# Kernel optimization log

Hardware: AMD Instinct MI355X
Metric: run time of the kernel (lower is better)

The kernel has to match this reference:

```python
import jax, jax.numpy as jnp
import numpy as np

EPS = 1e-3


def interpolate_dim(x, n_out):
    # linear interpolation along axis 1, align_corners=True (matches F.interpolate linear)
    n_in = x.shape[1]
    pos = jnp.linspace(0.0, n_in - 1.0, n_out)
    idx0 = jnp.floor(pos).astype(jnp.int32)
    idx1 = jnp.minimum(idx0 + 1, n_in - 1)
    w = (pos - idx0.astype(x.dtype))[None, :, None]
    return x[:, idx0] * (1.0 - w) + x[:, idx1] * w


def logits_to_a_coeff(a_logits, eps):
    # stability-triangle parameterization: |a1| < 2, |a1| - 1 < a2 < 1
    stab = 1.0 - eps
    a1 = 2.0 * jnp.tanh(a_logits[..., 0]) * stab
    a1_abs = jnp.abs(a1)
    a2 = 0.5 * ((2.0 - a1_abs) * jnp.tanh(a_logits[..., 1]) * stab + a1_abs)
    return jnp.stack([a1, a2], axis=-1)  # (B, T, 2)


def sample_wise_lpc(x, a_coeff):
    # time-varying all-pole: y[t] = x[t] - a1[t]*y[t-1] - a2[t]*y[t-2]
    bs = x.shape[0]
    xs = (x.T, a_coeff[..., 0].T, a_coeff[..., 1].T)  # (T, B) each

    def step(carry, inp):
        y1, y2 = carry
        xt, a1, a2 = inp
        y = xt - a1 * y1 - a2 * y2
        return (y, y1), y

    zero = jnp.zeros((bs,), x.dtype)
    _, ys = jax.lax.scan(step, (zero, zero), xs)
    return ys.T  # (B, T)


def time_varying_fir(y, b_coeff):
    # y_out[t] = b0[t]*y[t] + b1[t]*y[t-1] + b2[t]*y[t-2], zero initial conditions
    y_pad = jnp.pad(y, ((0, 0), (2, 0)))
    return (b_coeff[..., 0] * y
            + b_coeff[..., 1] * y_pad[:, 1:-1]
            + b_coeff[..., 2] * y_pad[:, :-2])


def setup_inputs() -> dict:
    key = jax.random.key(0)
    k1, k2 = jax.random.split(key)
    x = jax.random.normal(k1, (32, 262144), dtype=jnp.float32)
    coeff_logits = jax.random.normal(k2, (32, 256, 5), dtype=jnp.float32)
    return {"x": x, "coeff_logits": coeff_logits}


def reference(x, coeff_logits):
    n_samples = x.shape[1]
    # interp_coeff=False: interpolate logits to sample rate first
    logits = interpolate_dim(coeff_logits, n_samples)  # (B, n_samples, 5)
    a_coeff = logits_to_a_coeff(logits[..., :2], EPS)  # (B, n_samples, 2)
    b_coeff = logits[..., 2:]                          # (B, n_samples, 3)
    y_a = sample_wise_lpc(x, a_coeff)
    y_ab = time_varying_fir(y_a, b_coeff)
    return y_ab
```

## Files before the change

### kernel.cpp

```cpp
#include <hip/hip_runtime.h>
#include <math.h>

#define BATCH 32
#define NSAMP 262144
#define NKNOT 256
#define EPSV  0.001f
#define CH    16
#define CPB   256
#define NCROW (NSAMP / CH)
#define BPR   (NCROW / CPB)
#define NB    (BATCH * BPR)
#define TC    (NB * CPB)
#define NWAVE (CPB / 64)

__device__ __forceinline__ float fast_tanh(float x) {
    float e = __expf(2.0f * x);
    float r = __builtin_amdgcn_rcpf(e + 1.0f);
    return fmaf(-2.0f, r, 1.0f);
}

__global__ __launch_bounds__(256, 4) void k_agg(
    const float* __restrict__ x,
    const float* __restrict__ cl,
    float* __restrict__ Cb,
    float* __restrict__ G)
{
    __shared__ float wag[NWAVE][6];
    const int tid = threadIdx.x;
    const int b = blockIdx.x;
    const int lane = tid & 63, wid = tid >> 6;

    int chunk = b * CPB + tid;
    const float4* xp = (const float4*)(x + (size_t)chunk * CH);

    int r = chunk >> 14;
    int c = chunk & (NCROW - 1);
    const float scale = 255.0f / 262143.0f;
    float pos0 = (float)(c * CH) * scale;
    float fiA = floorf(pos0);
    int idxA = (int)fiA;
    float w0v = pos0 - fiA;
    const float* kb = cl + (size_t)r * NKNOT * 5;
    int i1 = min(idxA + 1, NKNOT - 1);
    int i2 = min(idxA + 2, NKNOT - 1);
    float k00 = kb[idxA*5+0], k01 = kb[i1*5+0], k02 = kb[i2*5+0];
    float k10 = kb[idxA*5+1], k11 = kb[i1*5+1], k12 = kb[i2*5+1];
    float d0A = k01-k00, d0B = k02-k01;
    float d1A = k11-k10, d1B = k12-k11;

    const float stab = 1.0f - EPSV, stab2 = 2.0f * stab;
    float p1 = 0.f, p2 = 0.f, A1 = 1.f, A2 = 0.f, B1 = 0.f, B2 = 1.f;
    #pragma unroll
    for (int v4 = 0; v4 < 4; ++v4) {
        float4 xq = xp[v4];
        #pragma unroll
        for (int q = 0; q < 4; ++q) {
            int j = v4 * 4 + q;
            float w = fmaf((float)j, scale, w0v);
            bool sel = w >= 1.0f;
            float wu = sel ? w - 1.0f : w;
            float l0 = fmaf(wu, sel ? d0B : d0A, sel ? k01 : k00);
            float l1 = fmaf(wu, sel ? d1B : d1A, sel ? k11 : k10);
            float a1 = stab2 * fast_tanh(l0);
            float a1a = fabsf(a1);
            float a2 = 0.5f * fmaf((2.0f - a1a) * stab, fast_tanh(l1), a1a);
            float p  = fmaf(-a2, p2, (&xq.x)[q]);  p = fmaf(-a1, p1, p);
            float hA = fmaf(-a1, A1, -a2 * A2);
            float hB = fmaf(-a1, B1, -a2 * B2);
            p2 = p1; p1 = p;
            A2 = A1; A1 = hA;
            B2 = B1; B1 = hB;
        }
    }
    float L00 = A1, L01 = B1, L10 = A2, L11 = B2, Lv0 = p1, Lv1 = p2;

    #pragma unroll
    for (int d = 1; d < 64; d <<= 1) {
        float o00 = __shfl_up(L00, d), o01 = __shfl_up(L01, d);
        float o10 = __shfl_up(L10, d), o11 = __shfl_up(L11, d);
        float ov0 = __shfl_up(Lv0, d), ov1 = __shfl_up(Lv1, d);
        if (lane >= d) {
            float n00 = L00 * o00 + L01 * o10;
            float n01 = L00 * o01 + L01 * o11;
            float n10 = L10 * o00 + L11 * o10;
            float n11 = L10 * o01 + L11 * o11;
            float nv0 = fmaf(L00, ov0, fmaf(L01, ov1, Lv0));
            float nv1 = fmaf(L10, ov0, fmaf(L11, ov1, Lv1));
            L00 = n00; L01 = n01; L10 = n10; L11 = n11; Lv0 = nv0; Lv1 = nv1;
        }
    }
    if (lane == 63) {
        wag[wid][0] = L00; wag[wid][1] = L01; wag[wid][2] = L10;
        wag[wid][3] = L11; wag[wid][4] = Lv0; wag[wid][5] = Lv1;
    }
    __syncthreads();

    float P00 = 1.f, P01 = 0.f, P10 = 0.f, P11 = 1.f, Pv0 = 0.f, Pv1 = 0.f;
    for (int w2 = 0; w2 < wid; ++w2) {
        float a00 = wag[w2][0], a01 = wag[w2][1], a10 = wag[w2][2];
        float a11 = wag[w2][3], av0 = wag[w2][4], av1 = wag[w2][5];
        float n00 = a00 * P00 + a01 * P10;
        float n01 = a00 * P01 + a01 * P11;
        float n10 = a10 * P00 + a11 * P10;
        float n11 = a10 * P01 + a11 * P11;
        float nv0 = fmaf(a00, Pv0, fmaf(a01, Pv1, av0));
        float nv1 = fmaf(a10, Pv0, fmaf(a11, Pv1, av1));
        P00 = n00; P01 = n01; P10 = n10; P11 = n11; Pv0 = nv0; Pv1 = nv1;
    }
    float E00 = __shfl_up(L00, 1), E01 = __shfl_up(L01, 1);
    float E10 = __shfl_up(L10, 1), E11 = __shfl_up(L11, 1);
    float Ev0 = __shfl_up(Lv0, 1), Ev1 = __shfl_up(Lv1, 1);
    if (lane == 0) { E00 = 1.f; E01 = 0.f; E10 = 0.f; E11 = 1.f; Ev0 = 0.f; Ev1 = 0.f; }
    Cb[0*TC + chunk] = E00 * P00 + E01 * P10;
    Cb[1*TC + chunk] = E00 * P01 + E01 * P11;
    Cb[2*TC + chunk] = E10 * P00 + E11 * P10;
    Cb[3*TC + chunk] = E10 * P01 + E11 * P11;
    Cb[4*TC + chunk] = fmaf(E00, Pv0, fmaf(E01, Pv1, Ev0));
    Cb[5*TC + chunk] = fmaf(E10, Pv0, fmaf(E11, Pv1, Ev1));

    if (tid == CPB - 1) {
        G[0*NB + b] = L00 * P00 + L01 * P10;
        G[1*NB + b] = L00 * P01 + L01 * P11;
        G[2*NB + b] = L10 * P00 + L11 * P10;
        G[3*NB + b] = L10 * P01 + L11 * P11;
        G[4*NB + b] = fmaf(L00, Pv0, fmaf(L01, Pv1, Lv0));
        G[5*NB + b] = fmaf(L10, Pv0, fmaf(L11, Pv1, Lv1));
    }
}

__global__ __launch_bounds__(256, 6) void k_apply(
    const float* __restrict__ x,
    const float* __restrict__ cl,
    const float* __restrict__ Cb,
    const float* __restrict__ G,
    float* __restrict__ out)
{
    __shared__ float sInit[2];
    const int tid = threadIdx.x;
    const int b = blockIdx.x;
    const int lane = tid & 63, wid = tid >> 6;

    if (wid == 0) {
        int rowFirst = b & ~(BPR - 1);
        int k = rowFirst + lane;
        float A00 = G[0*NB + k], A01 = G[1*NB + k], A10 = G[2*NB + k];
        float A11 = G[3*NB + k], Av0 = G[4*NB + k], Av1 = G[5*NB + k];
        #pragma unroll
        for (int d = 1; d < 64; d <<= 1) {
            float o00 = __shfl_up(A00, d), o01 = __shfl_up(A01, d);
            float o10 = __shfl_up(A10, d), o11 = __shfl_up(A11, d);
            float ov0 = __shfl_up(Av0, d), ov1 = __shfl_up(Av1, d);
            if (lane >= d) {
                float n00 = A00 * o00 + A01 * o10;
                float n01 = A00 * o01 + A01 * o11;
                float n10 = A10 * o00 + A11 * o10;
                float n11 = A10 * o01 + A11 * o11;
                float nv0 = fmaf(A00, ov0, fmaf(A01, ov1, Av0));
                float nv1 = fmaf(A10, ov0, fmaf(A11, ov1, Av1));
                A00 = n00; A01 = n01; A10 = n10; A11 = n11; Av0 = nv0; Av1 = nv1;
            }
        }
        int myIdx = b & (BPR - 1);
        int src = (myIdx > 0) ? myIdx - 1 : 0;
        float s0 = __shfl(Av0, src);
        float s1 = __shfl(Av1, src);
        if (lane == 0) {
            sInit[0] = myIdx ? s0 : 0.f;
            sInit[1] = myIdx ? s1 : 0.f;
        }
    }

    int chunk = b * CPB + tid;
    int r = chunk >> 14;
    int c = chunk & (NCROW - 1);
    const float scale = 255.0f / 262143.0f;
    float pos0 = (float)(c * CH) * scale;
    float fiA = floorf(pos0);
    int idxA = (int)fiA;
    float w0v = pos0 - fiA;
    const float* kb = cl + (size_t)r * NKNOT * 5;
    int i1 = min(idxA + 1, NKNOT - 1);
    int i2 = min(idxA + 2, NKNOT - 1);
    float k00 = kb[idxA*5+0], k01 = kb[i1*5+0], k02 = kb[i2*5+0];
    float k10 = kb[idxA*5+1], k11 = kb[i1*5+1], k12 = kb[i2*5+1];
    float k20 = kb[idxA*5+2], k21 = kb[i1*5+2], k22 = kb[i2*5+2];
    float k30 = kb[idxA*5+3], k31 = kb[i1*5+3], k32 = kb[i2*5+3];
    float k40 = kb[idxA*5+4], k41 = kb[i1*5+4], k42 = kb[i2*5+4];
    float d0A = k01-k00, d0B = k02-k01;
    float d1A = k11-k10, d1B = k12-k11;
    float d2A = k21-k20, d2B = k22-k21;
    float d3A = k31-k30, d3B = k32-k31;
    float d4A = k41-k40, d4B = k42-k41;

    float C00 = Cb[0*TC + chunk], C01 = Cb[1*TC + chunk];
    float C10 = Cb[2*TC + chunk], C11 = Cb[3*TC + chunk];
    float Cv0 = Cb[4*TC + chunk], Cv1 = Cb[5*TC + chunk];

    __syncthreads();
    float s0 = sInit[0], s1 = sInit[1];
    float y1 = fmaf(C00, s0, fmaf(C01, s1, Cv0));
    float y2 = fmaf(C10, s0, fmaf(C11, s1, Cv1));

    const float stab = 1.0f - EPSV, stab2 = 2.0f * stab;
    const float4* xp = (const float4*)(x + (size_t)chunk * CH);
    float4* op = (float4*)(out + (size_t)chunk * CH);
    #pragma unroll
    for (int v4 = 0; v4 < 4; ++v4) {
        float4 xq = xp[v4];
        float4 ov;
        #pragma unroll
        for (int q = 0; q < 4; ++q) {
            int j = v4 * 4 + q;
            float w = fmaf((float)j, scale, w0v);
            bool sel = w >= 1.0f;
            float wu = sel ? w - 1.0f : w;
            float l0 = fmaf(wu, sel ? d0B : d0A, sel ? k01 : k00);
            float l1 = fmaf(wu, sel ? d1B : d1A, sel ? k11 : k10);
            float b0 = fmaf(wu, sel ? d2B : d2A, sel ? k21 : k20);
            float b1c= fmaf(wu, sel ? d3B : d3A, sel ? k31 : k30);
            float b2c= fmaf(wu, sel ? d4B : d4A, sel ? k41 : k40);
            float a1 = stab2 * fast_tanh(l0);
            float a1a = fabsf(a1);
            float a2 = 0.5f * fmaf((2.0f - a1a) * stab, fast_tanh(l1), a1a);
            float y = fmaf(-a2, y2, (&xq.x)[q]);  y = fmaf(-a1, y1, y);
            (&ov.x)[q] = fmaf(b0, y, fmaf(b1c, y1, b2c * y2));
            y2 = y1; y1 = y;
        }
        op[v4] = ov;
    }
}

extern "C" void kernel_launch(void* const* d_in, const int* in_sizes, int n_in,
                              void* d_out, int out_size, void* d_ws, size_t ws_size,
                              hipStream_t stream) {
    const float* x  = (const float*)d_in[0];
    const float* cl = (const float*)d_in[1];
    float* out = (float*)d_out;
    float* Cb = (float*)d_ws;
    float* G  = Cb + (size_t)6 * TC;

    hipLaunchKernelGGL(k_agg,   dim3(NB), dim3(CPB), 0, stream, x, cl, Cb, G);
    hipLaunchKernelGGL(k_apply, dim3(NB), dim3(CPB), 0, stream, x, cl, Cb, G, out);
}
```

Measured before the change: 38.95 us.

## Process two chunks per thread in aggregation and redistribute scan blocks

The aggregation kernel now has each thread handle two adjacent 16-sample chunks. It composes their transfer matrices locally before the wave scan, so each block covers 512 chunks and half as many blocks are launched. Both chunks' carry-in states are written as float2 pairs. The apply kernel uses 512-thread blocks whose every wave redundantly scans the 32 per-row block aggregates with shuffles, which removes the shared-memory broadcast and the __syncthreads. This trades more per-thread register pressure and ILP in the aggregation kernel for fewer scan levels and less synchronization, but it halves parallelism in k_agg.

```diff
diff --git a/kernel.cpp b/kernel.cpp
--- a/kernel.cpp
+++ b/kernel.cpp
@@ -6,12 +6,11 @@
 #define NKNOT 256
 #define EPSV  0.001f
 #define CH    16
-#define CPB   256
 #define NCROW (NSAMP / CH)
-#define BPR   (NCROW / CPB)
-#define NB    (BATCH * BPR)
-#define TC    (NB * CPB)
-#define NWAVE (CPB / 64)
+#define CPBLK 512
+#define BPRB  (NCROW / CPBLK)
+#define NBLK  (BATCH * NCROW / CPBLK)
+#define TC    (BATCH * NCROW)
 
 __device__ __forceinline__ float fast_tanh(float x) {
     float e = __expf(2.0f * x);
@@ -25,54 +24,91 @@
     float* __restrict__ Cb,
     float* __restrict__ G)
 {
-    __shared__ float wag[NWAVE][6];
+    __shared__ float wag[4][6];
     const int tid = threadIdx.x;
     const int b = blockIdx.x;
     const int lane = tid & 63, wid = tid >> 6;
 
-    int chunk = b * CPB + tid;
-    const float4* xp = (const float4*)(x + (size_t)chunk * CH);
-
-    int r = chunk >> 14;
-    int c = chunk & (NCROW - 1);
+    const int chunk0 = b * CPBLK + 2 * tid;
+    const float4* xp = (const float4*)(x + (size_t)chunk0 * CH);
+
     const float scale = 255.0f / 262143.0f;
-    float pos0 = (float)(c * CH) * scale;
-    float fiA = floorf(pos0);
-    int idxA = (int)fiA;
-    float w0v = pos0 - fiA;
+    int r = chunk0 >> 14;
     const float* kb = cl + (size_t)r * NKNOT * 5;
-    int i1 = min(idxA + 1, NKNOT - 1);
-    int i2 = min(idxA + 2, NKNOT - 1);
-    float k00 = kb[idxA*5+0], k01 = kb[i1*5+0], k02 = kb[i2*5+0];
-    float k10 = kb[idxA*5+1], k11 = kb[i1*5+1], k12 = kb[i2*5+1];
-    float d0A = k01-k00, d0B = k02-k01;
-    float d1A = k11-k10, d1B = k12-k11;
+
+    int cA = chunk0 & (NCROW - 1);
+    float posA = (float)(cA * CH) * scale;
+    float fiA = floorf(posA);
+    int iA0 = (int)fiA;
+    float wA = posA - fiA;
+    int iA1 = min(iA0 + 1, NKNOT - 1), iA2 = min(iA0 + 2, NKNOT - 1);
+    float a_k00 = kb[iA0*5+0], a_k01 = kb[iA1*5+0], a_k02 = kb[iA2*5+0];
+    float a_k10 = kb[iA0*5+1], a_k11 = kb[iA1*5+1], a_k12 = kb[iA2*5+1];
+    float a_d0A = a_k01-a_k00, a_d0B = a_k02-a_k01;
+    float a_d1A = a_k11-a_k10, a_d1B = a_k12-a_k11;
+
+    int cB = cA + 1;
+    float posB = (float)(cB * CH) * scale;
+    float fiB = floorf(posB);
+    int iB0 = (int)fiB;
+    float wB = posB - fiB;
+    int iB1 = min(iB0 + 1, NKNOT - 1), iB2 = min(iB0 + 2, NKNOT - 1);
+    float b_k00 = kb[iB0*5+0], b_k01 = kb[iB1*5+0], b_k02 = kb[iB2*5+0];
+    float b_k10 = kb[iB0*5+1], b_k11 = kb[iB1*5+1], b_k12 = kb[iB2*5+1];
+    float b_d0A = b_k01-b_k00, b_d0B = b_k02-b_k01;
+    float b_d1A = b_k11-b_k10, b_d1B = b_k12-b_k11;
 
     const float stab = 1.0f - EPSV, stab2 = 2.0f * stab;
-    float p1 = 0.f, p2 = 0.f, A1 = 1.f, A2 = 0.f, B1 = 0.f, B2 = 1.f;
+    float ap1 = 0.f, ap2 = 0.f, aA1 = 1.f, aA2 = 0.f, aB1 = 0.f, aB2 = 1.f;
+    float bp1 = 0.f, bp2 = 0.f, bA1 = 1.f, bA2 = 0.f, bB1 = 0.f, bB2 = 1.f;
     #pragma unroll
     for (int v4 = 0; v4 < 4; ++v4) {
-        float4 xq = xp[v4];
+        float4 xqa = xp[v4];
+        float4 xqb = xp[4 + v4];
         #pragma unroll
         for (int q = 0; q < 4; ++q) {
             int j = v4 * 4 + q;
-            float w = fmaf((float)j, scale, w0v);
-            bool sel = w >= 1.0f;
-            float wu = sel ? w - 1.0f : w;
-            float l0 = fmaf(wu, sel ? d0B : d0A, sel ? k01 : k00);
-            float l1 = fmaf(wu, sel ? d1B : d1A, sel ? k11 : k10);
-            float a1 = stab2 * fast_tanh(l0);
-            float a1a = fabsf(a1);
-            float a2 = 0.5f * fmaf((2.0f - a1a) * stab, fast_tanh(l1), a1a);
-            float p  = fmaf(-a2, p2, (&xq.x)[q]);  p = fmaf(-a1, p1, p);
-            float hA = fmaf(-a1, A1, -a2 * A2);
-            float hB = fmaf(-a1, B1, -a2 * B2);
-            p2 = p1; p1 = p;
-            A2 = A1; A1 = hA;
-            B2 = B1; B1 = hB;
-        }
-    }
-    float L00 = A1, L01 = B1, L10 = A2, L11 = B2, Lv0 = p1, Lv1 = p2;
+            {
+                float w = fmaf((float)j, scale, wA);
+                bool sel = w >= 1.0f;
+                float wu = sel ? w - 1.0f : w;
+                float l0 = fmaf(wu, sel ? a_d0B : a_d0A, sel ? a_k01 : a_k00);
+                float l1 = fmaf(wu, sel ? a_d1B : a_d1A, sel ? a_k11 : a_k10);
+                float a1 = stab2 * fast_tanh(l0);
+                float a1a = fabsf(a1);
+                float a2 = 0.5f * fmaf((2.0f - a1a) * stab, fast_tanh(l1), a1a);
+                float p  = fmaf(-a2, ap2, (&xqa.x)[q]);  p = fmaf(-a1, ap1, p);
+                float hA = fmaf(-a1, aA1, -a2 * aA2);
+                float hB = fmaf(-a1, aB1, -a2 * aB2);
+                ap2 = ap1; ap1 = p;
+                aA2 = aA1; aA1 = hA;
+                aB2 = aB1; aB1 = hB;
+            }
+            {
+                float w = fmaf((float)j, scale, wB);
+                bool sel = w >= 1.0f;
+                float wu = sel ? w - 1.0f : w;
+                float l0 = fmaf(wu, sel ? b_d0B : b_d0A, sel ? b_k01 : b_k00);
+                float l1 = fmaf(wu, sel ? b_d1B : b_d1A, sel ? b_k11 : b_k10);
+                float a1 = stab2 * fast_tanh(l0);
+                float a1a = fabsf(a1);
+                float a2 = 0.5f * fmaf((2.0f - a1a) * stab, fast_tanh(l1), a1a);
+                float p  = fmaf(-a2, bp2, (&xqb.x)[q]);  p = fmaf(-a1, bp1, p);
+                float hA = fmaf(-a1, bA1, -a2 * bA2);
+                float hB = fmaf(-a1, bB1, -a2 * bB2);
+                bp2 = bp1; bp1 = p;
+                bA2 = bA1; bA1 = hA;
+                bB2 = bB1; bB1 = hB;
+            }
+        }
+    }
+    float Ma00 = aA1, Ma01 = aB1, Ma10 = aA2, Ma11 = aB2, Mav0 = ap1, Mav1 = ap2;
+    float L00 = bA1*Ma00 + bB1*Ma10;
+    float L01 = bA1*Ma01 + bB1*Ma11;
+    float L10 = bA2*Ma00 + bB2*Ma10;
+    float L11 = bA2*Ma01 + bB2*Ma11;
+    float Lv0 = fmaf(bA1, Mav0, fmaf(bB1, Mav1, bp1));
+    float Lv1 = fmaf(bA2, Mav0, fmaf(bB2, Mav1, bp2));
 
     #pragma unroll
     for (int d = 1; d < 64; d <<= 1) {
@@ -111,66 +147,76 @@
     float E10 = __shfl_up(L10, 1), E11 = __shfl_up(L11, 1);
     float Ev0 = __shfl_up(Lv0, 1), Ev1 = __shfl_up(Lv1, 1);
     if (lane == 0) { E00 = 1.f; E01 = 0.f; E10 = 0.f; E11 = 1.f; Ev0 = 0.f; Ev1 = 0.f; }
-    Cb[0*TC + chunk] = E00 * P00 + E01 * P10;
-    Cb[1*TC + chunk] = E00 * P01 + E01 * P11;
-    Cb[2*TC + chunk] = E10 * P00 + E11 * P10;
-    Cb[3*TC + chunk] = E10 * P01 + E11 * P11;
-    Cb[4*TC + chunk] = fmaf(E00, Pv0, fmaf(E01, Pv1, Ev0));
-    Cb[5*TC + chunk] = fmaf(E10, Pv0, fmaf(E11, Pv1, Ev1));
-
-    if (tid == CPB - 1) {
-        G[0*NB + b] = L00 * P00 + L01 * P10;
-        G[1*NB + b] = L00 * P01 + L01 * P11;
-        G[2*NB + b] = L10 * P00 + L11 * P10;
-        G[3*NB + b] = L10 * P01 + L11 * P11;
-        G[4*NB + b] = fmaf(L00, Pv0, fmaf(L01, Pv1, Lv0));
-        G[5*NB + b] = fmaf(L10, Pv0, fmaf(L11, Pv1, Lv1));
-    }
-}
-
-__global__ __launch_bounds__(256, 6) void k_apply(
+    float C00 = E00 * P00 + E01 * P10;
+    float C01 = E00 * P01 + E01 * P11;
+    float C10 = E10 * P00 + E11 * P10;
+    float C11 = E10 * P01 + E11 * P11;
+    float Cv0 = fmaf(E00, Pv0, fmaf(E01, Pv1, Ev0));
+    float Cv1 = fmaf(E10, Pv0, fmaf(E11, Pv1, Ev1));
+    float D00 = Ma00 * C00 + Ma01 * C10;
+    float D01 = Ma00 * C01 + Ma01 * C11;
+    float D10 = Ma10 * C00 + Ma11 * C10;
+    float D11 = Ma10 * C01 + Ma11 * C11;
+    float Dv0 = fmaf(Ma00, Cv0, fmaf(Ma01, Cv1, Mav0));
+    float Dv1 = fmaf(Ma10, Cv0, fmaf(Ma11, Cv1, Mav1));
+
+    *(float2*)&Cb[0*TC + chunk0] = make_float2(C00, D00);
+    *(float2*)&Cb[1*TC + chunk0] = make_float2(C01, D01);
+    *(float2*)&Cb[2*TC + chunk0] = make_float2(C10, D10);
+    *(float2*)&Cb[3*TC + chunk0] = make_float2(C11, D11);
+    *(float2*)&Cb[4*TC + chunk0] = make_float2(Cv0, Dv0);
+    *(float2*)&Cb[5*TC + chunk0] = make_float2(Cv1, Dv1);
+
+    if (tid == 255) {
+        G[0*NBLK + b] = L00 * P00 + L01 * P10;
+        G[1*NBLK + b] = L00 * P01 + L01 * P11;
+        G[2*NBLK + b] = L10 * P00 + L11 * P10;
+        G[3*NBLK + b] = L10 * P01 + L11 * P11;
+        G[4*NBLK + b] = fmaf(L00, Pv0, fmaf(L01, Pv1, Lv0));
+        G[5*NBLK + b] = fmaf(L10, Pv0, fmaf(L11, Pv1, Lv1));
+    }
+}
+
+__global__ __launch_bounds__(512, 4) void k_apply(
     const float* __restrict__ x,
     const float* __restrict__ cl,
     const float* __restrict__ Cb,
     const float* __restrict__ G,
     float* __restrict__ out)
 {
-    __shared__ float sInit[2];
     const int tid = threadIdx.x;
     const int b = blockIdx.x;
-    const int lane = tid & 63, wid = tid >> 6;
-
-    if (wid == 0) {
-        int rowFirst = b & ~(BPR - 1);
+    const int lane = tid & 63;
+
+    const int myIdx = b & (BPRB - 1);
+    const int rowFirst = b - myIdx;
+    float A00 = 1.f, A01 = 0.f, A10 = 0.f, A11 = 1.f, Av0 = 0.f, Av1 = 0.f;
+    if (lane < BPRB) {
         int k = rowFirst + lane;
-        float A00 = G[0*NB + k], A01 = G[1*NB + k], A10 = G[2*NB + k];
-        float A11 = G[3*NB + k], Av0 = G[4*NB + k], Av1 = G[5*NB + k];
-        #pragma unroll
-        for (int d = 1; d < 64; d <<= 1) {
-            float o00 = __shfl_up(A00, d), o01 = __shfl_up(A01, d);
-            float o10 = __shfl_up(A10, d), o11 = __shfl_up(A11, d);
-            float ov0 = __shfl_up(Av0, d), ov1 = __shfl_up(Av1, d);
-            if (lane >= d) {
-                float n00 = A00 * o00 + A01 * o10;
-                float n01 = A00 * o01 + A01 * o11;
-                float n10 = A10 * o00 + A11 * o10;
-                float n11 = A10 * o01 + A11 * o11;
-                float nv0 = fmaf(A00, ov0, fmaf(A01, ov1, Av0));
-                float nv1 = fmaf(A10, ov0, fmaf(A11, ov1, Av1));
-                A00 = n00; A01 = n01; A10 = n10; A11 = n11; Av0 = nv0; Av1 = nv1;
-            }
-        }
-        int myIdx = b & (BPR - 1);
-        int src = (myIdx > 0) ? myIdx - 1 : 0;
-        float s0 = __shfl(Av0, src);
-        float s1 = __shfl(Av1, src);
-        if (lane == 0) {
-            sInit[0] = myIdx ? s0 : 0.f;
-            sInit[1] = myIdx ? s1 : 0.f;
-        }
-    }
-
-    int chunk = b * CPB + tid;
+        A00 = G[0*NBLK + k]; A01 = G[1*NBLK + k]; A10 = G[2*NBLK + k];
+        A11 = G[3*NBLK + k]; Av0 = G[4*NBLK + k]; Av1 = G[5*NBLK + k];
+    }
+    #pragma unroll
+    for (int d = 1; d < BPRB; d <<= 1) {
+        float o00 = __shfl_up(A00, d), o01 = __shfl_up(A01, d);
+        float o10 = __shfl_up(A10, d), o11 = __shfl_up(A11, d);
+        float ov0 = __shfl_up(Av0, d), ov1 = __shfl_up(Av1, d);
+        if (lane >= d) {
+            float n00 = A00 * o00 + A01 * o10;
+            float n01 = A00 * o01 + A01 * o11;
+            float n10 = A10 * o00 + A11 * o10;
+            float n11 = A10 * o01 + A11 * o11;
+            float nv0 = fmaf(A00, ov0, fmaf(A01, ov1, Av0));
+            float nv1 = fmaf(A10, ov0, fmaf(A11, ov1, Av1));
+            A00 = n00; A01 = n01; A10 = n10; A11 = n11; Av0 = nv0; Av1 = nv1;
+        }
+    }
+    int src = (myIdx > 0) ? myIdx - 1 : 0;
+    float s0 = __shfl(Av0, src);
+    float s1 = __shfl(Av1, src);
+    if (myIdx == 0) { s0 = 0.f; s1 = 0.f; }
+
+    int chunk = b * CPBLK + tid;
     int r = chunk >> 14;
     int c = chunk & (NCROW - 1);
     const float scale = 255.0f / 262143.0f;
@@ -195,9 +241,6 @@
     float C00 = Cb[0*TC + chunk], C01 = Cb[1*TC + chunk];
     float C10 = Cb[2*TC + chunk], C11 = Cb[3*TC + chunk];
     float Cv0 = Cb[4*TC + chunk], Cv1 = Cb[5*TC + chunk];
-
-    __syncthreads();
-    float s0 = sInit[0], s1 = sInit[1];
     float y1 = fmaf(C00, s0, fmaf(C01, s1, Cv0));
     float y2 = fmaf(C10, s0, fmaf(C11, s1, Cv1));
 
@@ -239,6 +282,6 @@
     float* Cb = (float*)d_ws;
     float* G  = Cb + (size_t)6 * TC;
 
-    hipLaunchKernelGGL(k_agg,   dim3(NB), dim3(CPB), 0, stream, x, cl, Cb, G);
-    hipLaunchKernelGGL(k_apply, dim3(NB), dim3(CPB), 0, stream, x, cl, Cb, G, out);
-}
+    hipLaunchKernelGGL(k_agg,   dim3(NBLK), dim3(256), 0, stream, x, cl, Cb, G);
+    hipLaunchKernelGGL(k_apply, dim3(NBLK), dim3(512), 0, stream, x, cl, Cb, G, out);
+}
```

New measurement: 40.61 us. +4.3%, slower.

## Process two chunks per thread in apply kernel and drop shared-memory sync

Applied to the files above, without the earlier changes.

The apply kernel now gives each thread two adjacent chunks and interleaves their two serial recurrences, which raises instruction-level parallelism on the latency-bound filter chain. The block count is halved. Every wave now redoes the 64-lane scan of block aggregates and reads its own carry-in with a shuffle, so the LDS broadcast and the __syncthreads are gone. In exchange it uses more registers (occupancy hint lowered from 6 to 4), repeats the scan in every wave, and widens the per-thread memory stride.

```diff
diff --git a/kernel.cpp b/kernel.cpp
--- a/kernel.cpp
+++ b/kernel.cpp
@@ -9,8 +9,8 @@
 #define CPB   256
 #define NCROW (NSAMP / CH)
 #define BPR   (NCROW / CPB)
-#define NB    (BATCH * BPR)
-#define TC    (NB * CPB)
+#define NB    (BATCH * NCROW / CPB)
+#define TC    (BATCH * NCROW)
 #define NWAVE (CPB / 64)
 
 __device__ __forceinline__ float fast_tanh(float x) {
@@ -128,21 +128,20 @@
     }
 }
 
-__global__ __launch_bounds__(256, 6) void k_apply(
+__global__ __launch_bounds__(256, 4) void k_apply(
     const float* __restrict__ x,
     const float* __restrict__ cl,
     const float* __restrict__ Cb,
     const float* __restrict__ G,
     float* __restrict__ out)
 {
-    __shared__ float sInit[2];
     const int tid = threadIdx.x;
     const int b = blockIdx.x;
-    const int lane = tid & 63, wid = tid >> 6;
-
-    if (wid == 0) {
-        int rowFirst = b & ~(BPR - 1);
-        int k = rowFirst + lane;
+    const int lane = tid & 63;
+
+    const int rowFirstAgg = (b >> 5) * BPR;
+    {
+        int k = rowFirstAgg + lane;
         float A00 = G[0*NB + k], A01 = G[1*NB + k], A10 = G[2*NB + k];
         float A11 = G[3*NB + k], Av0 = G[4*NB + k], Av1 = G[5*NB + k];
         #pragma unroll
@@ -160,73 +159,101 @@
                 A00 = n00; A01 = n01; A10 = n10; A11 = n11; Av0 = nv0; Av1 = nv1;
             }
         }
-        int myIdx = b & (BPR - 1);
-        int src = (myIdx > 0) ? myIdx - 1 : 0;
-        float s0 = __shfl(Av0, src);
-        float s1 = __shfl(Av1, src);
-        if (lane == 0) {
-            sInit[0] = myIdx ? s0 : 0.f;
-            sInit[1] = myIdx ? s1 : 0.f;
-        }
-    }
-
-    int chunk = b * CPB + tid;
-    int r = chunk >> 14;
-    int c = chunk & (NCROW - 1);
-    const float scale = 255.0f / 262143.0f;
-    float pos0 = (float)(c * CH) * scale;
-    float fiA = floorf(pos0);
-    int idxA = (int)fiA;
-    float w0v = pos0 - fiA;
-    const float* kb = cl + (size_t)r * NKNOT * 5;
-    int i1 = min(idxA + 1, NKNOT - 1);
-    int i2 = min(idxA + 2, NKNOT - 1);
-    float k00 = kb[idxA*5+0], k01 = kb[i1*5+0], k02 = kb[i2*5+0];
-    float k10 = kb[idxA*5+1], k11 = kb[i1*5+1], k12 = kb[i2*5+1];
-    float k20 = kb[idxA*5+2], k21 = kb[i1*5+2], k22 = kb[i2*5+2];
-    float k30 = kb[idxA*5+3], k31 = kb[i1*5+3], k32 = kb[i2*5+3];
-    float k40 = kb[idxA*5+4], k41 = kb[i1*5+4], k42 = kb[i2*5+4];
-    float d0A = k01-k00, d0B = k02-k01;
-    float d1A = k11-k10, d1B = k12-k11;
-    float d2A = k21-k20, d2B = k22-k21;
-    float d3A = k31-k30, d3B = k32-k31;
-    float d4A = k41-k40, d4B = k42-k41;
-
-    float C00 = Cb[0*TC + chunk], C01 = Cb[1*TC + chunk];
-    float C10 = Cb[2*TC + chunk], C11 = Cb[3*TC + chunk];
-    float Cv0 = Cb[4*TC + chunk], Cv1 = Cb[5*TC + chunk];
-
-    __syncthreads();
-    float s0 = sInit[0], s1 = sInit[1];
-    float y1 = fmaf(C00, s0, fmaf(C01, s1, Cv0));
-    float y2 = fmaf(C10, s0, fmaf(C11, s1, Cv1));
-
-    const float stab = 1.0f - EPSV, stab2 = 2.0f * stab;
-    const float4* xp = (const float4*)(x + (size_t)chunk * CH);
-    float4* op = (float4*)(out + (size_t)chunk * CH);
-    #pragma unroll
-    for (int v4 = 0; v4 < 4; ++v4) {
-        float4 xq = xp[v4];
-        float4 ov;
-        #pragma unroll
-        for (int q = 0; q < 4; ++q) {
-            int j = v4 * 4 + q;
-            float w = fmaf((float)j, scale, w0v);
-            bool sel = w >= 1.0f;
-            float wu = sel ? w - 1.0f : w;
-            float l0 = fmaf(wu, sel ? d0B : d0A, sel ? k01 : k00);
-            float l1 = fmaf(wu, sel ? d1B : d1A, sel ? k11 : k10);
-            float b0 = fmaf(wu, sel ? d2B : d2A, sel ? k21 : k20);
-            float b1c= fmaf(wu, sel ? d3B : d3A, sel ? k31 : k30);
-            float b2c= fmaf(wu, sel ? d4B : d4A, sel ? k41 : k40);
-            float a1 = stab2 * fast_tanh(l0);
-            float a1a = fabsf(a1);
-            float a2 = 0.5f * fmaf((2.0f - a1a) * stab, fast_tanh(l1), a1a);
-            float y = fmaf(-a2, y2, (&xq.x)[q]);  y = fmaf(-a1, y1, y);
-            (&ov.x)[q] = fmaf(b0, y, fmaf(b1c, y1, b2c * y2));
-            y2 = y1; y1 = y;
-        }
-        op[v4] = ov;
+        int idxInRow = ((b & 31) << 1) + (tid >> 7);
+        float t0 = __shfl(Av0, idxInRow - 1);
+        float t1 = __shfl(Av1, idxInRow - 1);
+        Av0 = (idxInRow > 0) ? t0 : 0.f;
+        Av1 = (idxInRow > 0) ? t1 : 0.f;
+        A00 = Av0; A01 = Av1;
+        #define S0_ A00
+        #define S1_ A01
+        const int chunk0 = b * 512 + 2 * tid;
+        const float scale = 255.0f / 262143.0f;
+        int r = chunk0 >> 14;
+        const float* kb = cl + (size_t)r * NKNOT * 5;
+
+        int cA = chunk0 & (NCROW - 1);
+        float posA = (float)(cA * CH) * scale;
+        float fiA = floorf(posA);
+        int iA0 = (int)fiA;
+        float wA0 = posA - fiA;
+        int iA1 = min(iA0 + 1, NKNOT - 1), iA2 = min(iA0 + 2, NKNOT - 1);
+        float ak0[5], ak1[5], ak2[5];
+        #pragma unroll
+        for (int ch2 = 0; ch2 < 5; ++ch2) {
+            ak0[ch2] = kb[iA0*5+ch2]; ak1[ch2] = kb[iA1*5+ch2]; ak2[ch2] = kb[iA2*5+ch2];
+        }
+        float posB = (float)((cA + 1) * CH) * scale;
+        float fiB = floorf(posB);
+        int iB0 = (int)fiB;
+        float wB0 = posB - fiB;
+        int iB1 = min(iB0 + 1, NKNOT - 1), iB2 = min(iB0 + 2, NKNOT - 1);
+        float bk0[5], bk1[5], bk2[5];
+        #pragma unroll
+        for (int ch2 = 0; ch2 < 5; ++ch2) {
+            bk0[ch2] = kb[iB0*5+ch2]; bk1[ch2] = kb[iB1*5+ch2]; bk2[ch2] = kb[iB2*5+ch2];
+        }
+
+        float2 c0 = *(const float2*)&Cb[0*TC + chunk0];
+        float2 c1 = *(const float2*)&Cb[1*TC + chunk0];
+        float2 c2 = *(const float2*)&Cb[2*TC + chunk0];
+        float2 c3 = *(const float2*)&Cb[3*TC + chunk0];
+        float2 c4 = *(const float2*)&Cb[4*TC + chunk0];
+        float2 c5 = *(const float2*)&Cb[5*TC + chunk0];
+        float yA1 = fmaf(c0.x, S0_, fmaf(c1.x, S1_, c4.x));
+        float yA2 = fmaf(c2.x, S0_, fmaf(c3.x, S1_, c5.x));
+        float yB1 = fmaf(c0.y, S0_, fmaf(c1.y, S1_, c4.y));
+        float yB2 = fmaf(c2.y, S0_, fmaf(c3.y, S1_, c5.y));
+
+        const float stab = 1.0f - EPSV, stab2 = 2.0f * stab;
+        const float4* xp = (const float4*)(x + (size_t)chunk0 * CH);
+        float4* op = (float4*)(out + (size_t)chunk0 * CH);
+        #pragma unroll
+        for (int v4 = 0; v4 < 4; ++v4) {
+            float4 xqa = xp[v4];
+            float4 xqb = xp[4 + v4];
+            float4 ova, ovb;
+            #pragma unroll
+            for (int q = 0; q < 4; ++q) {
+                int j = v4 * 4 + q;
+                {
+                    float w = fmaf((float)j, scale, wA0);
+                    bool sel = w >= 1.0f;
+                    float wu = sel ? w - 1.0f : w;
+                    float l0 = fmaf(wu, sel ? ak2[0]-ak1[0] : ak1[0]-ak0[0], sel ? ak1[0] : ak0[0]);
+                    float l1 = fmaf(wu, sel ? ak2[1]-ak1[1] : ak1[1]-ak0[1], sel ? ak1[1] : ak0[1]);
+                    float b0 = fmaf(wu, sel ? ak2[2]-ak1[2] : ak1[2]-ak0[2], sel ? ak1[2] : ak0[2]);
+                    float b1c= fmaf(wu, sel ? ak2[3]-ak1[3] : ak1[3]-ak0[3], sel ? ak1[3] : ak0[3]);
+                    float b2c= fmaf(wu, sel ? ak2[4]-ak1[4] : ak1[4]-ak0[4], sel ? ak1[4] : ak0[4]);
+                    float a1 = stab2 * fast_tanh(l0);
+                    float a1a = fabsf(a1);
+                    float a2 = 0.5f * fmaf((2.0f - a1a) * stab, fast_tanh(l1), a1a);
+                    float y = fmaf(-a2, yA2, (&xqa.x)[q]);  y = fmaf(-a1, yA1, y);
+                    (&ova.x)[q] = fmaf(b0, y, fmaf(b1c, yA1, b2c * yA2));
+                    yA2 = yA1; yA1 = y;
+                }
+                {
+                    float w = fmaf((float)j, scale, wB0);
+                    bool sel = w >= 1.0f;
+                    float wu = sel ? w - 1.0f : w;
+                    float l0 = fmaf(wu, sel ? bk2[0]-bk1[0] : bk1[0]-bk0[0], sel ? bk1[0] : bk0[0]);
+                    float l1 = fmaf(wu, sel ? bk2[1]-bk1[1] : bk1[1]-bk0[1], sel ? bk1[1] : bk0[1]);
+                    float b0 = fmaf(wu, sel ? bk2[2]-bk1[2] : bk1[2]-bk0[2], sel ? bk1[2] : bk0[2]);
+                    float b1c= fmaf(wu, sel ? bk2[3]-bk1[3] : bk1[3]-bk0[3], sel ? bk1[3] : bk0[3]);
+                    float b2c= fmaf(wu, sel ? bk2[4]-bk1[4] : bk1[4]-bk0[4], sel ? bk1[4] : bk0[4]);
+                    float a1 = stab2 * fast_tanh(l0);
+                    float a1a = fabsf(a1);
+                    float a2 = 0.5f * fmaf((2.0f - a1a) * stab, fast_tanh(l1), a1a);
+                    float y = fmaf(-a2, yB2, (&xqb.x)[q]);  y = fmaf(-a1, yB1, y);
+                    (&ovb.x)[q] = fmaf(b0, y, fmaf(b1c, yB1, b2c * yB2));
+                    yB2 = yB1; yB1 = y;
+                }
+            }
+            op[v4] = ova;
+            op[4 + v4] = ovb;
+        }
+        #undef S0_
+        #undef S1_
     }
 }
 
@@ -239,6 +266,6 @@
     float* Cb = (float*)d_ws;
     float* G  = Cb + (size_t)6 * TC;
 
-    hipLaunchKernelGGL(k_agg,   dim3(NB), dim3(CPB), 0, stream, x, cl, Cb, G);
-    hipLaunchKernelGGL(k_apply, dim3(NB), dim3(CPB), 0, stream, x, cl, Cb, G, out);
-}
+    hipLaunchKernelGGL(k_agg,   dim3(NB),     dim3(256), 0, stream, x, cl, Cb, G);
+    hipLaunchKernelGGL(k_apply, dim3(TC/512), dim3(256), 0, stream, x, cl, Cb, G, out);
+}
```

Result: slower. 58.04 us (+49.0%).
